# Performance work log

Measured on AMD Instinct MI355X. Metric: run time of the kernel, lower is better.

Reference implementation:

```python
import jax, jax.numpy as jnp
import numpy as np

DIM = 384; HEADS = 6; POINTS = 4; LEVELS = 3; HID = 96
B = 2; D0 = 12; H0 = 12; W0 = 12
NMID = D0 * H0 * W0          # mid-level tokens
NTOK = 73 * NMID // 8        # total tokens across 3 scales


def _ln(x, w, b, eps=1e-6):
    m = x.mean(-1, keepdims=True)
    v = ((x - m) ** 2).mean(-1, keepdims=True)
    return (x - m) * jax.lax.rsqrt(v + eps) * w + b


def _make_ref(shapes):
    # matches get_reference_points: per-level normalized centers, stacked as (d, x, y)
    refs = []
    for (D_, H_, W_) in shapes:
        d = (jnp.arange(D_, dtype=jnp.float32) + 0.5) / D_
        y = (jnp.arange(H_, dtype=jnp.float32) + 0.5) / H_
        x = (jnp.arange(W_, dtype=jnp.float32) + 0.5) / W_
        dd, yy, xx = jnp.meshgrid(d, y, x, indexing='ij')
        refs.append(jnp.stack([dd.ravel(), xx.ravel(), yy.ravel()], -1))
    return jnp.concatenate(refs, 0)[None, :, None, :]  # [1, N, 1, 3]


def _sample_level(v, D_, H_, W_, loc):
    # v: [B,S,h,hd]; loc: [B,Nq,h,P,3] normalized (d,x,y); trilinear, zero padding,
    # align_corners=False semantics (pixel = norm*size - 0.5)
    Bq, Nq, h, P, _ = loc.shape
    hd = v.shape[-1]
    pd = loc[..., 0] * D_ - 0.5
    px = loc[..., 1] * W_ - 0.5
    py = loc[..., 2] * H_ - 0.5
    d0 = jnp.floor(pd); x0 = jnp.floor(px); y0 = jnp.floor(py)
    fd = pd - d0; fx = px - x0; fy = py - y0
    d0 = d0.astype(jnp.int32); x0 = x0.astype(jnp.int32); y0 = y0.astype(jnp.int32)
    acc = jnp.zeros((Bq, Nq, h, P, hd), v.dtype)
    for dd in (0, 1):  # fixed 8-corner loop
        for dy in (0, 1):
            for dx in (0, 1):
                di = d0 + dd; yi = y0 + dy; xi = x0 + dx
                wgt = (fd if dd else 1.0 - fd) * (fy if dy else 1.0 - fy) * (fx if dx else 1.0 - fx)
                valid = ((di >= 0) & (di < D_) & (yi >= 0) & (yi < H_) & (xi >= 0) & (xi < W_)).astype(v.dtype)
                idx = (jnp.clip(di, 0, D_ - 1) * H_ + jnp.clip(yi, 0, H_ - 1)) * W_ + jnp.clip(xi, 0, W_ - 1)
                idx_t = idx.transpose(0, 1, 3, 2).reshape(Bq, Nq * P, h)
                g = jnp.take_along_axis(v, idx_t[..., None], axis=1)  # [B,Nq*P,h,hd]
                g = g.reshape(Bq, Nq, P, h, hd).transpose(0, 1, 3, 2, 4)
                acc = acc + (wgt * valid)[..., None] * g
    return acc  # [B,Nq,h,P,hd]


def _msdeform(q, ref, feat, shapes, off_w, off_b, aw_w, aw_b, val_w, val_b, out_w, out_b):
    Bq, Nq, C = q.shape
    hd = C // HEADS
    value = (feat @ val_w + val_b).reshape(Bq, -1, HEADS, hd)
    off = (q @ off_w + off_b).reshape(Bq, Nq, HEADS, LEVELS, POINTS, 3)
    aw = jax.nn.softmax((q @ aw_w + aw_b).reshape(Bq, Nq, HEADS, LEVELS * POINTS), -1)
    aw = aw.reshape(Bq, Nq, HEADS, LEVELS, POINTS)
    # offset normalizer in (d, x, y) order -> (D, W, H)
    norm = jnp.array([[D_, W_, H_] for (D_, H_, W_) in shapes], dtype=q.dtype)
    loc = ref[:, :, None, :, None, :] + off / norm[None, None, None, :, None, :]
    out = jnp.zeros((Bq, Nq, HEADS, hd), q.dtype)
    start = 0
    for l, (D_, H_, W_) in enumerate(shapes):
        S = D_ * H_ * W_
        sampled = _sample_level(value[:, start:start + S], D_, H_, W_, loc[:, :, :, l])
        out = out + jnp.einsum('bqhp,bqhpd->bqhd', aw[:, :, :, l], sampled)
        start += S
    return out.reshape(Bq, Nq, C) @ out_w + out_b


def _dwconv_seg(x, Dv, Hv, Wv, w, b):
    Bq, S, C = x.shape
    xv = x.reshape(Bq, Dv, Hv, Wv, C)
    y = jax.lax.conv_general_dilated(xv, w, (1, 1, 1), 'SAME',
                                     dimension_numbers=('NDHWC', 'DHWIO', 'NDHWC'),
                                     feature_group_count=C) + b
    return y.reshape(Bq, S, C)


def _conv_ffn(x, D, H, W, fc1_w, fc1_b, dw_w, dw_b, fc2_w, fc2_b):
    x = x @ fc1_w + fc1_b
    n = x.shape[1] // 73
    x1 = _dwconv_seg(x[:, :64 * n], 2 * D, 2 * H, 2 * W, dw_w, dw_b)
    x2 = _dwconv_seg(x[:, 64 * n:72 * n], D, H, W, dw_w, dw_b)
    x3 = _dwconv_seg(x[:, 72 * n:], D // 2, H // 2, W // 2, dw_w, dw_b)
    x = jax.nn.gelu(jnp.concatenate([x1, x2, x3], 1), approximate=False)
    return x @ fc2_w + fc2_b


def _forward(query, feat, D, H, W,
             qnorm_w, qnorm_b, fnorm_w, fnorm_b, ext_qnorm_w, ext_qnorm_b,
             ext_fnorm_w, ext_fnorm_b, ffn_norm_w, ffn_norm_b,
             off_w, off_b, aw_w, aw_b, val_w, val_b, out_w, out_b,
             fc1_w, fc1_b, dw_w, dw_b, fc2_w, fc2_b):
    n_mid = D * H * W
    n_high = 8 * n_mid
    x2 = query[:, n_high:n_high + n_mid] + feat
    q = jnp.concatenate([query[:, :n_high], x2, query[:, n_high + n_mid:]], 1)
    shapes = [(2 * D, 2 * H, 2 * W), (D, H, W), (D // 2, H // 2, W // 2)]
    ref = _make_ref(shapes)
    qn = _ln(q, qnorm_w, qnorm_b)      # CTI_toC.query_norm
    fn = _ln(q, fnorm_w, fnorm_b)      # CTI_toC.feat_norm
    aq = _ln(qn, ext_qnorm_w, ext_qnorm_b)  # MultiscaleExtractor.query_norm
    af = _ln(fn, ext_fnorm_w, ext_fnorm_b)  # MultiscaleExtractor.feat_norm
    out = qn + _msdeform(aq, ref, af, shapes, off_w, off_b, aw_w, aw_b, val_w, val_b, out_w, out_b)
    out = out + _conv_ffn(_ln(out, ffn_norm_w, ffn_norm_b), D, H, W,
                          fc1_w, fc1_b, dw_w, dw_b, fc2_w, fc2_b)
    return out


def setup_inputs() -> dict:
    key = jax.random.key(0)
    ks = jax.random.split(key, 16)
    w = lambda k, *s: jax.random.normal(k, s, jnp.float32) * 0.02
    NO = HEADS * LEVELS * POINTS * 3
    NA = HEADS * LEVELS * POINTS
    return {
        'query': jax.random.normal(ks[0], (B, NTOK, DIM), jnp.float32),
        'reference_points': jax.random.uniform(ks[1], (1, NTOK, 1, 3), dtype=jnp.float32),
        'feat': jax.random.normal(ks[2], (B, NMID, DIM), jnp.float32),
        'spatial_shapes': jnp.array([[2 * D0, 2 * H0, 2 * W0], [D0, H0, W0], [D0 // 2, H0 // 2, W0 // 2]], jnp.int32),
        'level_start_index': jnp.array([0, 8 * NMID, 9 * NMID], jnp.int32),
        'D': D0, 'H': H0, 'W': W0,
        'qnorm_w': jnp.ones(DIM), 'qnorm_b': jnp.zeros(DIM),
        'fnorm_w': jnp.ones(DIM), 'fnorm_b': jnp.zeros(DIM),
        'ext_qnorm_w': jnp.ones(DIM), 'ext_qnorm_b': jnp.zeros(DIM),
        'ext_fnorm_w': jnp.ones(DIM), 'ext_fnorm_b': jnp.zeros(DIM),
        'ffn_norm_w': jnp.ones(DIM), 'ffn_norm_b': jnp.zeros(DIM),
        'off_w': w(ks[3], DIM, NO), 'off_b': jnp.zeros(NO),
        'aw_w': w(ks[4], DIM, NA), 'aw_b': jnp.zeros(NA),
        'val_w': w(ks[5], DIM, DIM), 'val_b': jnp.zeros(DIM),
        'out_w': w(ks[6], DIM, DIM), 'out_b': jnp.zeros(DIM),
        'fc1_w': w(ks[7], DIM, HID), 'fc1_b': jnp.zeros(HID),
        'dw_w': w(ks[8], 3, 3, 3, 1, HID), 'dw_b': jnp.zeros(HID),
        'fc2_w': w(ks[9], HID, DIM), 'fc2_b': jnp.zeros(DIM),
    }


def reference(query, reference_points, feat, spatial_shapes, level_start_index, D, H, W,
              qnorm_w, qnorm_b, fnorm_w, fnorm_b, ext_qnorm_w, ext_qnorm_b,
              ext_fnorm_w, ext_fnorm_b, ffn_norm_w, ffn_norm_b,
              off_w, off_b, aw_w, aw_b, val_w, val_b, out_w, out_b,
              fc1_w, fc1_b, dw_w, dw_b, fc2_w, fc2_b):
    # reference_points / spatial_shapes / level_start_index are required by the torch
    # signature but unused: CTI_toC recomputes deform inputs internally.
    return _forward(query, feat, D, H, W,
                    qnorm_w, qnorm_b, fnorm_w, fnorm_b, ext_qnorm_w, ext_qnorm_b,
                    ext_fnorm_w, ext_fnorm_b, ffn_norm_w, ffn_norm_b,
                    off_w, off_b, aw_w, aw_b, val_w, val_b, out_w, out_b,
                    fc1_w, fc1_b, dw_w, dw_b, fc2_w, fc2_b)
```

## Files before the change

### kernel.cpp

```cpp
#include <hip/hip_runtime.h>
#include <hip/hip_fp16.h>
#include <cstdint>
#include <cstddef>

#define DIM    384
#define HEADS  6
#define HD     64
#define NTOK   15768
#define NMID   1728
#define BATCH  2
#define ROWS   (BATCH*NTOK)
#define MPAD   31616
#define L1START 13824
#define L2START 15552
#define HID    96
#define VROWS  (ROWS + 8)
#define VSLAB  ((size_t)VROWS * 64)

typedef __attribute__((ext_vector_type(8))) short short8;
typedef __attribute__((ext_vector_type(4))) float floatx4;

__device__ __forceinline__ unsigned short f2bf(float x){
  unsigned u = __float_as_uint(x);
  unsigned r = (u + 0x7FFFu + ((u >> 16) & 1u)) >> 16;
  return (unsigned short)r;
}

__device__ __forceinline__ float wave_sum(float v){
  #pragma unroll
  for (int o = 32; o; o >>= 1) v += __shfl_xor(v, o, 64);
  return v;
}

__device__ __forceinline__ void ln384(const float* x, float* y,
                                      const float* __restrict__ w,
                                      const float* __restrict__ b, int lane){
  float s = 0.f;
  #pragma unroll
  for (int j = 0; j < 6; j++) s += x[j];
  s = wave_sum(s);
  float m = s * (1.f/384.f);
  float v = 0.f;
  #pragma unroll
  for (int j = 0; j < 6; j++){ float d = x[j] - m; v += d*d; }
  v = wave_sum(v) * (1.f/384.f);
  float rs = rsqrtf(v + 1e-6f);
  #pragma unroll
  for (int j = 0; j < 6; j++){
    int c = j*64 + lane;
    y[j] = (x[j] - m) * rs * w[c] + b[c];
  }
}

__global__ void k_ln_front(const float* __restrict__ query, const float* __restrict__ feat,
                           const float* __restrict__ qw,  const float* __restrict__ qb,
                           const float* __restrict__ fw,  const float* __restrict__ fb,
                           const float* __restrict__ eqw, const float* __restrict__ eqb,
                           const float* __restrict__ efw, const float* __restrict__ efb,
                           float* __restrict__ qn, unsigned short* __restrict__ aq,
                           unsigned short* __restrict__ af){
  int wid = blockIdx.x * (blockDim.x >> 6) + (threadIdx.x >> 6);
  if (wid >= ROWS) return;
  int lane = threadIdx.x & 63;
  int b = wid / NTOK, t = wid - b*NTOK;
  const float* qp = query + (size_t)wid * DIM;
  float x[6];
  #pragma unroll
  for (int j = 0; j < 6; j++) x[j] = qp[j*64 + lane];
  if (t >= L1START && t < L2START){
    const float* fp = feat + ((size_t)b*NMID + (t - L1START)) * DIM;
    #pragma unroll
    for (int j = 0; j < 6; j++) x[j] += fp[j*64 + lane];
  }
  float y[6], z[6];
  ln384(x, y, qw, qb, lane);
  {
    float* o = qn + (size_t)wid * DIM;
    #pragma unroll
    for (int j = 0; j < 6; j++) o[j*64 + lane] = y[j];
  }
  ln384(y, z, eqw, eqb, lane);
  {
    unsigned short* o = aq + (size_t)wid * DIM;
    #pragma unroll
    for (int j = 0; j < 6; j++) o[j*64 + lane] = f2bf(z[j]);
  }
  ln384(x, y, fw, fb, lane);
  ln384(y, z, efw, efb, lane);
  {
    unsigned short* o = af + (size_t)wid * DIM;
    #pragma unroll
    for (int j = 0; j < 6; j++) o[j*64 + lane] = f2bf(z[j]);
  }
}

__global__ void k_ln(const float* __restrict__ in, const float* __restrict__ w,
                     const float* __restrict__ b, unsigned short* __restrict__ out){
  int wid = blockIdx.x * (blockDim.x >> 6) + (threadIdx.x >> 6);
  if (wid >= ROWS) return;
  int lane = threadIdx.x & 63;
  float x[6], y[6];
  const float* p = in + (size_t)wid * DIM;
  #pragma unroll
  for (int j = 0; j < 6; j++) x[j] = p[j*64 + lane];
  ln384(x, y, w, b, lane);
  unsigned short* o = out + (size_t)wid * DIM;
  #pragma unroll
  for (int j = 0; j < 6; j++) o[j*64 + lane] = f2bf(y[j]);
}

__global__ void k_cvt_all(const float* __restrict__ val_w, const float* __restrict__ off_w,
                          const float* __restrict__ aw_w,  const float* __restrict__ out_w,
                          const float* __restrict__ fc1_w, const float* __restrict__ fc2_w,
                          const float* __restrict__ off_b, const float* __restrict__ aw_b,
                          unsigned short* __restrict__ wt_val, unsigned short* __restrict__ wt_offaw,
                          unsigned short* __restrict__ wt_out, unsigned short* __restrict__ wt_fc1,
                          unsigned short* __restrict__ wt_fc2, float* __restrict__ offaw_b){
  int id = blockIdx.x * blockDim.x + threadIdx.x;
  if (id < 147456){
    int n = id / 384, k = id - n*384;
    wt_val[id] = f2bf(val_w[(size_t)k*384 + n]);
  } else if (id < 294912){
    int i = id - 147456;
    int n = i / 384, k = i - n*384;
    float v = 0.f;
    if (n < 216) v = off_w[(size_t)k*216 + n];
    else if (n >= 256 && n < 328) v = aw_w[(size_t)k*72 + (n-256)];
    wt_offaw[i] = f2bf(v);
  } else if (id < 442368){
    int i = id - 294912;
    int n = i / 384, k = i - n*384;
    wt_out[i] = f2bf(out_w[(size_t)k*384 + n]);
  } else if (id < 491520){
    int i = id - 442368;
    int n = i / 384, k = i - n*384;
    wt_fc1[i] = f2bf((n < 96) ? fc1_w[(size_t)k*96 + n] : 0.f);
  } else if (id < 528384){
    int i = id - 491520;
    int n = i / 96, k = i - n*96;
    wt_fc2[i] = f2bf(fc2_w[(size_t)k*384 + n]);
  } else if (id < 528768){
    int n = id - 528384;
    float v = 0.f;
    if (n < 216) v = off_b[n];
    else if (n >= 256 && n < 328) v = aw_b[n-256];
    offaw_b[n] = v;
  }
}

template<int OUTMODE>
__global__ __launch_bounds__(256) void k_gemm(
    const unsigned short* __restrict__ A,
    const unsigned short* __restrict__ Wt,
    const float* __restrict__ bias,
    const float* __restrict__ R,
    void* __restrict__ Cv,
    int M, int N, int K){
  __shared__ __align__(16) unsigned short As[128*32];
  __shared__ __align__(16) unsigned short Bs[128*32];
  int tid = threadIdx.x;
  int w = tid >> 6, lane = tid & 63;
  int m0 = blockIdx.y * 128, n0 = blockIdx.x * 128;
  int m_off = (w & 1) * 64, n_off = (w >> 1) * 64;

  floatx4 acc[4][4] = {};

  int sr = lane >> 2;
  int sc = (lane & 3) * 8;
  int lrow = lane & 15;
  int kq = (lane >> 4) * 8;

  for (int k0 = 0; k0 < K; k0 += 32){
    #pragma unroll
    for (int s = 0; s < 2; s++){
      int c = w * 2 + s;
      const unsigned short* ga = A  + (size_t)(m0 + c*16 + sr) * K + k0 + sc;
      __builtin_amdgcn_global_load_lds(
          (const __attribute__((address_space(1))) void*)ga,
          (__attribute__((address_space(3))) void*)(As + c*512), 16, 0, 0);
      const unsigned short* gb = Wt + (size_t)(n0 + c*16 + sr) * K + k0 + sc;
      __builtin_amdgcn_global_load_lds(
          (const __attribute__((address_space(1))) void*)gb,
          (__attribute__((address_space(3))) void*)(Bs + c*512), 16, 0, 0);
    }
    __syncthreads();
    short8 afr[4], bfr[4];
    #pragma unroll
    for (int i = 0; i < 4; i++)
      afr[i] = *(const short8*)(As + (m_off + i*16 + lrow)*32 + kq);
    #pragma unroll
    for (int j = 0; j < 4; j++)
      bfr[j] = *(const short8*)(Bs + (n_off + j*16 + lrow)*32 + kq);
    #pragma unroll
    for (int i = 0; i < 4; i++)
      #pragma unroll
      for (int j = 0; j < 4; j++)
        acc[i][j] = __builtin_amdgcn_mfma_f32_16x16x32_bf16(afr[i], bfr[j], acc[i][j], 0, 0, 0);
    __syncthreads();
  }

  int cn = n0 + n_off + lrow;
  int rbase = m0 + m_off + (lane >> 4) * 4;
  #pragma unroll
  for (int j = 0; j < 4; j++){
    int n = cn + j*16;
    if (n >= N) continue;
    float bj = bias[n];
    #pragma unroll
    for (int i = 0; i < 4; i++){
      int mb = rbase + i*16;
      #pragma unroll
      for (int r = 0; r < 4; r++){
        int m = mb + r;
        if (m < M){
          float v = acc[i][j][r] + bj;
          if (R) v += R[(size_t)m * N + n];
          if (OUTMODE == 0)      ((float*)Cv)[(size_t)m * N + n] = v;
          else if (OUTMODE == 1) ((unsigned short*)Cv)[(size_t)m * N + n] = f2bf(v);
          else {
            ((__half*)Cv)[(size_t)(n >> 6) * VSLAB + (size_t)m * 64 + (n & 63)] =
                __float2half_rn(v);
          }
        }
      }
    }
  }
}

__global__ __launch_bounds__(384) void k_msdeform(const __half* __restrict__ vt,
                                                  const float* __restrict__ offaw,
                                                  unsigned short* __restrict__ msout){
  int bx = blockIdx.x;
  int r = (bx & 7) * (ROWS/8) + (bx >> 3);
  int head = threadIdx.x >> 6;
  int lane = threadIdx.x & 63;
  int b = (r >= NTOK) ? 1 : 0;
  int t = r - b * NTOK;

  float refd, refy, refx;
  if (t < L1START){
    int i = t;
    int dd = i / 576; int rem = i - dd*576; int yy = rem / 24; int xx = rem - yy*24;
    refd = (dd + 0.5f) * (1.f/24.f); refy = (yy + 0.5f) * (1.f/24.f); refx = (xx + 0.5f) * (1.f/24.f);
  } else if (t < L2START){
    int i = t - L1START;
    int dd = i / 144; int rem = i - dd*144; int yy = rem / 12; int xx = rem - yy*12;
    refd = (dd + 0.5f) * (1.f/12.f); refy = (yy + 0.5f) * (1.f/12.f); refx = (xx + 0.5f) * (1.f/12.f);
  } else {
    int i = t - L2START;
    int dd = i / 36; int rem = i - dd*36; int yy = rem / 6; int xx = rem - yy*6;
    refd = (dd + 0.5f) * (1.f/6.f); refy = (yy + 0.5f) * (1.f/6.f); refx = (xx + 0.5f) * (1.f/6.f);
  }

  float logit = (lane < 12) ? offaw[(size_t)r * 384 + 256 + head * 12 + lane] : -1e30f;
  float mx = logit;
  mx = fmaxf(mx, __shfl_xor(mx, 1));
  mx = fmaxf(mx, __shfl_xor(mx, 2));
  mx = fmaxf(mx, __shfl_xor(mx, 4));
  mx = fmaxf(mx, __shfl_xor(mx, 8));
  float e = (lane < 12) ? __expf(logit - mx) : 0.f;
  float s = e;
  s += __shfl_xor(s, 1);
  s += __shfl_xor(s, 2);
  s += __shfl_xor(s, 4);
  s += __shfl_xor(s, 8);
  float aww = e / s;
  float awwj = __shfl(aww, lane >> 2, 64);

  int rowk = 0, wgtk = 0;
  if (lane < 48){
    int j = lane >> 2, p = lane & 3;
    int l = j >> 2;
    int Dl  = (l == 0) ? 24 : ((l == 1) ? 12 : 6);
    int lst = (l == 0) ? 0  : ((l == 1) ? L1START : L2START);
    const float* op = offaw + (size_t)r * 384 + head * 36 + j * 3;
    float od = op[0], ox = op[1], oy = op[2];
    float fDl = (float)Dl;
    float pd = refd * fDl + od - 0.5f;
    float px = refx * fDl + ox - 0.5f;
    float py = refy * fDl + oy - 0.5f;
    float fld = floorf(pd), flx = floorf(px), fly = floorf(py);
    float fd = pd - fld, fx = px - flx, fy = py - fly;
    int d0 = (int)fld, x0 = (int)flx, y0 = (int)fly;
    int cz = p >> 1, cy = p & 1;
    int di = d0 + cz, yi = y0 + cy;
    bool vzy = (di >= 0) & (di < Dl) & (yi >= 0) & (yi < Dl);
    float wz = cz ? fd : 1.f - fd;
    float wy = cy ? fy : 1.f - fy;
    float wp = vzy ? (wz * awwj) * wy : 0.f;
    int rs = min(max(x0, 0), Dl - 1);
    float wlo_x = (rs == x0) ? (1.f - fx) : ((rs == x0 + 1) ? fx : 0.f);
    float whi_x = ((rs == x0) && (x0 + 1 < Dl)) ? fx : 0.f;
    int dc = min(max(di, 0), Dl - 1);
    int yc = min(max(yi, 0), Dl - 1);
    rowk = (b * NTOK + lst) + (dc * Dl + yc) * Dl + rs;
    __half2 wh = __floats2half2_rn(wp * wlo_x, wp * whi_x);
    wgtk = *(int*)&wh;
  }

  int grp = lane >> 4;
  unsigned selperm = (lane & 8) ? 0x03020302u : 0x01000100u;
  int rowv[12]; unsigned wsel[12];
  #pragma unroll
  for (int j = 0; j < 12; j++){
    rowv[j] = __shfl(rowk, j*4 + grp, 64);
    unsigned wj = (unsigned)__shfl(wgtk, j*4 + grp, 64);
    wsel[j] = __builtin_amdgcn_perm(wj, wj, selperm);
  }

  int head_u = __builtin_amdgcn_readfirstlane(head);
  const char* vbase = (const char*)(vt + (size_t)head_u * VSLAB);
  unsigned laneoff = (unsigned)(lane & 15) << 4;

  __half2 hz; *(int*)&hz = 0;
  __half2 a0 = hz, a1 = hz, a2 = hz, a3 = hz;
  #pragma unroll
  for (int j = 0; j < 12; j++){
    unsigned off = ((unsigned)rowv[j] << 7) + laneoff;
    uint4 v = *(const uint4*)(vbase + off);
    __half2 wh = *(__half2*)&wsel[j];
    a0 = __hfma2(wh, *(__half2*)&v.x, a0);
    a1 = __hfma2(wh, *(__half2*)&v.y, a1);
    a2 = __hfma2(wh, *(__half2*)&v.z, a2);
    a3 = __hfma2(wh, *(__half2*)&v.w, a3);
  }

  int i0 = *(int*)&a0, i1 = *(int*)&a1, i2 = *(int*)&a2, i3 = *(int*)&a3;
  int p0 = __shfl_xor(i0, 8, 64); int p1 = __shfl_xor(i1, 8, 64);
  int p2 = __shfl_xor(i2, 8, 64); int p3 = __shfl_xor(i3, 8, 64);
  a0 = __hadd2(a0, *(__half2*)&p0);
  a1 = __hadd2(a1, *(__half2*)&p1);
  a2 = __hadd2(a2, *(__half2*)&p2);
  a3 = __hadd2(a3, *(__half2*)&p3);
  float2 f0 = __half22float2(a0), f1 = __half22float2(a1);
  float2 f2 = __half22float2(a2), f3 = __half22float2(a3);
  float sv[8] = {f0.x, f0.y, f1.x, f1.y, f2.x, f2.y, f3.x, f3.y};
  #pragma unroll
  for (int k = 0; k < 8; k++){
    sv[k] += __shfl_xor(sv[k], 16, 64);
    sv[k] += __shfl_xor(sv[k], 32, 64);
  }

  if (lane < 8){
    uint4 pk;
    pk.x = ((unsigned)f2bf(sv[1]) << 16) | (unsigned)f2bf(sv[0]);
    pk.y = ((unsigned)f2bf(sv[3]) << 16) | (unsigned)f2bf(sv[2]);
    pk.z = ((unsigned)f2bf(sv[5]) << 16) | (unsigned)f2bf(sv[4]);
    pk.w = ((unsigned)f2bf(sv[7]) << 16) | (unsigned)f2bf(sv[6]);
    *(uint4*)(msout + (size_t)r * DIM + head * 64 + lane * 8) = pk;
  }
}

__global__ void k_dwconv_gelu(const float* __restrict__ h, const float* __restrict__ dww,
                              const float* __restrict__ dwb, unsigned short* __restrict__ h2){
  int gid = blockIdx.x * blockDim.x + threadIdx.x;
  if (gid >= ROWS * 24) return;
  int c4 = gid % 24;
  int r = gid / 24;
  int c = c4 * 4;
  int b = (r >= NTOK) ? 1 : 0;
  int t = r - b * NTOK;
  int base, DL, i;
  if (t < L1START){ base = 0; DL = 24; i = t; }
  else if (t < L2START){ base = L1START; DL = 12; i = t - L1START; }
  else { base = L2START; DL = 6; i = t - L2START; }
  int dd, yy, xx;
  if (DL == 24){ dd = i / 576; int rem = i - dd*576; yy = rem / 24; xx = rem - yy*24; }
  else if (DL == 12){ dd = i / 144; int rem = i - dd*144; yy = rem / 12; xx = rem - yy*12; }
  else { dd = i / 36; int rem = i - dd*36; yy = rem / 6; xx = rem - yy*6; }
  float4 acc = {0.f, 0.f, 0.f, 0.f};
  #pragma unroll
  for (int kz = 0; kz < 3; kz++){
    int nd = dd + kz - 1; if (nd < 0 || nd >= DL) continue;
    #pragma unroll
    for (int ky = 0; ky < 3; ky++){
      int ny = yy + ky - 1; if (ny < 0 || ny >= DL) continue;
      #pragma unroll
      for (int kx = 0; kx < 3; kx++){
        int nx = xx + kx - 1; if (nx < 0 || nx >= DL) continue;
        int nt = base + (nd * DL + ny) * DL + nx;
        float4 hv = *(const float4*)(h + ((size_t)(b*NTOK + nt)) * HID + c);
        float4 wv = *(const float4*)(dww + (size_t)((kz*3 + ky)*3 + kx) * HID + c);
        acc.x += hv.x * wv.x; acc.y += hv.y * wv.y;
        acc.z += hv.z * wv.z; acc.w += hv.w * wv.w;
      }
    }
  }
  float4 bv = *(const float4*)(dwb + c);
  acc.x += bv.x; acc.y += bv.y; acc.z += bv.z; acc.w += bv.w;
  const float k = 0.70710678118654752440f;
  float g0 = 0.5f * acc.x * (1.f + erff(acc.x * k));
  float g1 = 0.5f * acc.y * (1.f + erff(acc.y * k));
  float g2 = 0.5f * acc.z * (1.f + erff(acc.z * k));
  float g3 = 0.5f * acc.w * (1.f + erff(acc.w * k));
  uint2 pk;
  pk.x = ((unsigned)f2bf(g1) << 16) | (unsigned)f2bf(g0);
  pk.y = ((unsigned)f2bf(g3) << 16) | (unsigned)f2bf(g2);
  *(uint2*)(h2 + (size_t)r * HID + c) = pk;
}

extern "C" void kernel_launch(void* const* d_in, const int* in_sizes, int n_in,
                              void* d_out, int out_size, void* d_ws, size_t ws_size,
                              hipStream_t stream){
  const float* query = (const float*)d_in[0];
  const float* feat  = (const float*)d_in[2];
  const float* qnw = (const float*)d_in[8],  *qnb = (const float*)d_in[9];
  const float* fnw = (const float*)d_in[10], *fnb = (const float*)d_in[11];
  const float* eqw = (const float*)d_in[12], *eqb = (const float*)d_in[13];
  const float* efw = (const float*)d_in[14], *efb = (const float*)d_in[15];
  const float* ffw = (const float*)d_in[16], *ffb = (const float*)d_in[17];
  const float* off_w = (const float*)d_in[18], *off_b = (const float*)d_in[19];
  const float* aw_w  = (const float*)d_in[20], *aw_b  = (const float*)d_in[21];
  const float* val_w = (const float*)d_in[22], *val_b = (const float*)d_in[23];
  const float* out_w = (const float*)d_in[24], *out_b = (const float*)d_in[25];
  const float* fc1_w = (const float*)d_in[26], *fc1_b = (const float*)d_in[27];
  const float* dw_w  = (const float*)d_in[28], *dw_b  = (const float*)d_in[29];
  const float* fc2_w = (const float*)d_in[30], *fc2_b = (const float*)d_in[31];
  float* out = (float*)d_out;

  char* p = (char*)d_ws;
  float* qn             = (float*)p;          p += (size_t)ROWS*384*4;
  unsigned short* aq    = (unsigned short*)p; p += (size_t)MPAD*384*2;
  unsigned short* af    = (unsigned short*)p; p += (size_t)MPAD*384*2;
  __half* value_t       = (__half*)p;         p += (size_t)HEADS*VSLAB*2;
  float* offaw          = (float*)p;          p += (size_t)ROWS*384*4;
  unsigned short* wt_val   = (unsigned short*)p; p += (size_t)384*384*2;
  unsigned short* wt_offaw = (unsigned short*)p; p += (size_t)384*384*2;
  unsigned short* wt_out   = (unsigned short*)p; p += (size_t)384*384*2;
  unsigned short* wt_fc1   = (unsigned short*)p; p += (size_t)128*384*2;
  unsigned short* wt_fc2   = (unsigned short*)p; p += (size_t)384*96*2;
  float* offaw_b           = (float*)p;          p += (size_t)384*4;
  unsigned short* t_buf  = aq;
  unsigned short* msout  = af;
  float* y1              = offaw;
  float* h_buf           = (float*)value_t;
  unsigned short* h2_buf = (unsigned short*)qn;

  k_cvt_all<<<(528768 + 255)/256, 256, 0, stream>>>(val_w, off_w, aw_w, out_w, fc1_w, fc2_w,
                                                    off_b, aw_b,
                                                    wt_val, wt_offaw, wt_out, wt_fc1, wt_fc2,
                                                    offaw_b);

  int lnBlocks = ROWS / 4;
  k_ln_front<<<lnBlocks, 256, 0, stream>>>(query, feat, qnw, qnb, fnw, fnb,
                                           eqw, eqb, efw, efb, qn, aq, af);

  dim3 gN384(3, MPAD/128), gN128(1, MPAD/128);

  k_gemm<2><<<gN384, 256, 0, stream>>>(af, wt_val, val_b, nullptr, value_t, ROWS, 384, 384);
  k_gemm<0><<<gN384, 256, 0, stream>>>(aq, wt_offaw, offaw_b, nullptr, offaw, ROWS, 384, 384);
  k_msdeform<<<ROWS, 384, 0, stream>>>(value_t, offaw, msout);
  k_gemm<0><<<gN384, 256, 0, stream>>>(msout, wt_out, out_b, qn, y1, ROWS, 384, 384);
  k_ln<<<lnBlocks, 256, 0, stream>>>(y1, ffw, ffb, t_buf);
  k_gemm<0><<<gN128, 256, 0, stream>>>(t_buf, wt_fc1, fc1_b, nullptr, h_buf, ROWS, 96, 384);
  k_dwconv_gelu<<<(ROWS * 24 + 255)/256, 256, 0, stream>>>(h_buf, dw_w, dw_b, h2_buf);
  k_gemm<0><<<gN384, 256, 0, stream>>>(h2_buf, wt_fc2, fc2_b, y1, out, ROWS, 384, 96);
}
```

Measured before the change: 511.5 us.

## Restructure deformable sampling to one wave per head-row with swizzle-broadcast gathers

The deformable attention kernel changes from one 384-thread block per row to 64-thread blocks indexed by (head, row). Each lane now computes one sample point and corner, so the per-lane softmax shuffle goes away. Row indices and weights are broadcast with ds_swizzle, and all 12 gathers are issued up front before the FMAs. Packed bf16 conversion uses the v_cvt_pk_bf16_f32 instruction. The weight-convert kernel now zero-fills the value padding rows. The row interleaving used for locality is dropped, and the grid gets many more small blocks.

```diff
diff --git a/kernel.cpp b/kernel.cpp
--- a/kernel.cpp
+++ b/kernel.cpp
@@ -26,6 +26,12 @@
   return (unsigned short)r;
 }
 
+__device__ __forceinline__ unsigned cvt_pk_bf16(float lo, float hi){
+  unsigned r;
+  asm("v_cvt_pk_bf16_f32 %0, %1, %2" : "=v"(r) : "v"(lo), "v"(hi));
+  return r;
+}
+
 __device__ __forceinline__ float wave_sum(float v){
   #pragma unroll
   for (int o = 32; o; o >>= 1) v += __shfl_xor(v, o, 64);
@@ -115,7 +121,8 @@
                           const float* __restrict__ off_b, const float* __restrict__ aw_b,
                           unsigned short* __restrict__ wt_val, unsigned short* __restrict__ wt_offaw,
                           unsigned short* __restrict__ wt_out, unsigned short* __restrict__ wt_fc1,
-                          unsigned short* __restrict__ wt_fc2, float* __restrict__ offaw_b){
+                          unsigned short* __restrict__ wt_fc2, float* __restrict__ offaw_b,
+                          unsigned short* __restrict__ vt_pad){
   int id = blockIdx.x * blockDim.x + threadIdx.x;
   if (id < 147456){
     int n = id / 384, k = id - n*384;
@@ -145,6 +152,10 @@
     if (n < 216) v = off_b[n];
     else if (n >= 256 && n < 328) v = aw_b[n-256];
     offaw_b[n] = v;
+  } else if (id < 531840){
+    int i = id - 528768;
+    int hh = i >> 9, rem = i & 511;
+    vt_pad[(size_t)hh * VSLAB + (size_t)ROWS * 64 + rem] = 0;
   }
 }
 
@@ -227,12 +238,11 @@
   }
 }
 
-__global__ __launch_bounds__(384) void k_msdeform(const __half* __restrict__ vt,
-                                                  const float* __restrict__ offaw,
-                                                  unsigned short* __restrict__ msout){
-  int bx = blockIdx.x;
-  int r = (bx & 7) * (ROWS/8) + (bx >> 3);
-  int head = threadIdx.x >> 6;
+__global__ __launch_bounds__(64, 4) void k_msdeform(const __half* __restrict__ vt,
+                                                    const float* __restrict__ offaw,
+                                                    unsigned short* __restrict__ msout){
+  int head = blockIdx.x;
+  int r    = blockIdx.y;
   int lane = threadIdx.x & 63;
   int b = (r >= NTOK) ? 1 : 0;
   int t = r - b * NTOK;
@@ -252,24 +262,26 @@
     refd = (dd + 0.5f) * (1.f/6.f); refy = (yy + 0.5f) * (1.f/6.f); refx = (xx + 0.5f) * (1.f/6.f);
   }
 
-  float logit = (lane < 12) ? offaw[(size_t)r * 384 + 256 + head * 12 + lane] : -1e30f;
+  int s   = lane & 15;
+  int grp = lane >> 4;
+
+  float logit = (s < 12) ? offaw[(size_t)r * 384 + 256 + head * 12 + s] : -1e30f;
   float mx = logit;
-  mx = fmaxf(mx, __shfl_xor(mx, 1));
-  mx = fmaxf(mx, __shfl_xor(mx, 2));
-  mx = fmaxf(mx, __shfl_xor(mx, 4));
-  mx = fmaxf(mx, __shfl_xor(mx, 8));
-  float e = (lane < 12) ? __expf(logit - mx) : 0.f;
-  float s = e;
-  s += __shfl_xor(s, 1);
-  s += __shfl_xor(s, 2);
-  s += __shfl_xor(s, 4);
-  s += __shfl_xor(s, 8);
-  float aww = e / s;
-  float awwj = __shfl(aww, lane >> 2, 64);
+  mx = fmaxf(mx, __shfl_xor(mx, 1, 64));
+  mx = fmaxf(mx, __shfl_xor(mx, 2, 64));
+  mx = fmaxf(mx, __shfl_xor(mx, 4, 64));
+  mx = fmaxf(mx, __shfl_xor(mx, 8, 64));
+  float e = (s < 12) ? __expf(logit - mx) : 0.f;
+  float sum = e;
+  sum += __shfl_xor(sum, 1, 64);
+  sum += __shfl_xor(sum, 2, 64);
+  sum += __shfl_xor(sum, 4, 64);
+  sum += __shfl_xor(sum, 8, 64);
+  float aww = e / sum;
 
   int rowk = 0, wgtk = 0;
-  if (lane < 48){
-    int j = lane >> 2, p = lane & 3;
+  if (s < 12){
+    int j = s;
     int l = j >> 2;
     int Dl  = (l == 0) ? 24 : ((l == 1) ? 12 : 6);
     int lst = (l == 0) ? 0  : ((l == 1) ? L1START : L2START);
@@ -282,12 +294,12 @@
     float fld = floorf(pd), flx = floorf(px), fly = floorf(py);
     float fd = pd - fld, fx = px - flx, fy = py - fly;
     int d0 = (int)fld, x0 = (int)flx, y0 = (int)fly;
-    int cz = p >> 1, cy = p & 1;
+    int cz = grp >> 1, cy = grp & 1;
     int di = d0 + cz, yi = y0 + cy;
     bool vzy = (di >= 0) & (di < Dl) & (yi >= 0) & (yi < Dl);
     float wz = cz ? fd : 1.f - fd;
     float wy = cy ? fy : 1.f - fy;
-    float wp = vzy ? (wz * awwj) * wy : 0.f;
+    float wp = vzy ? (wz * aww) * wy : 0.f;
     int rs = min(max(x0, 0), Dl - 1);
     float wlo_x = (rs == x0) ? (1.f - fx) : ((rs == x0 + 1) ? fx : 0.f);
     float whi_x = ((rs == x0) && (x0 + 1 < Dl)) ? fx : 0.f;
@@ -298,27 +310,30 @@
     wgtk = *(int*)&wh;
   }
 
-  int grp = lane >> 4;
+  const char* vbase = (const char*)(vt + (size_t)head * VSLAB);
+  unsigned laneoff = (unsigned)(lane & 15) << 4;
   unsigned selperm = (lane & 8) ? 0x03020302u : 0x01000100u;
-  int rowv[12]; unsigned wsel[12];
-  #pragma unroll
-  for (int j = 0; j < 12; j++){
-    rowv[j] = __shfl(rowk, j*4 + grp, 64);
-    unsigned wj = (unsigned)__shfl(wgtk, j*4 + grp, 64);
-    wsel[j] = __builtin_amdgcn_perm(wj, wj, selperm);
-  }
-
-  int head_u = __builtin_amdgcn_readfirstlane(head);
-  const char* vbase = (const char*)(vt + (size_t)head_u * VSLAB);
-  unsigned laneoff = (unsigned)(lane & 15) << 4;
+
+  uint4 vd[12]; unsigned wv[12];
+  #define MS_LOAD(J) { int rw_ = __builtin_amdgcn_ds_swizzle(rowk, ((J) << 5) | 16); \
+    vd[J] = *(const uint4*)(vbase + ((((unsigned)rw_) << 7) + laneoff)); }
+  MS_LOAD(0)  MS_LOAD(1)  MS_LOAD(2)  MS_LOAD(3)
+  MS_LOAD(4)  MS_LOAD(5)  MS_LOAD(6)  MS_LOAD(7)
+  MS_LOAD(8)  MS_LOAD(9)  MS_LOAD(10) MS_LOAD(11)
+  #undef MS_LOAD
+  #define MS_W(J) { unsigned wj_ = (unsigned)__builtin_amdgcn_ds_swizzle(wgtk, ((J) << 5) | 16); \
+    wv[J] = __builtin_amdgcn_perm(wj_, wj_, selperm); }
+  MS_W(0)  MS_W(1)  MS_W(2)  MS_W(3)
+  MS_W(4)  MS_W(5)  MS_W(6)  MS_W(7)
+  MS_W(8)  MS_W(9)  MS_W(10) MS_W(11)
+  #undef MS_W
 
   __half2 hz; *(int*)&hz = 0;
   __half2 a0 = hz, a1 = hz, a2 = hz, a3 = hz;
   #pragma unroll
   for (int j = 0; j < 12; j++){
-    unsigned off = ((unsigned)rowv[j] << 7) + laneoff;
-    uint4 v = *(const uint4*)(vbase + off);
-    __half2 wh = *(__half2*)&wsel[j];
+    __half2 wh = *(__half2*)&wv[j];
+    uint4 v = vd[j];
     a0 = __hfma2(wh, *(__half2*)&v.x, a0);
     a1 = __hfma2(wh, *(__half2*)&v.y, a1);
     a2 = __hfma2(wh, *(__half2*)&v.z, a2);
@@ -343,10 +358,10 @@
 
   if (lane < 8){
     uint4 pk;
-    pk.x = ((unsigned)f2bf(sv[1]) << 16) | (unsigned)f2bf(sv[0]);
-    pk.y = ((unsigned)f2bf(sv[3]) << 16) | (unsigned)f2bf(sv[2]);
-    pk.z = ((unsigned)f2bf(sv[5]) << 16) | (unsigned)f2bf(sv[4]);
-    pk.w = ((unsigned)f2bf(sv[7]) << 16) | (unsigned)f2bf(sv[6]);
+    pk.x = cvt_pk_bf16(sv[0], sv[1]);
+    pk.y = cvt_pk_bf16(sv[2], sv[3]);
+    pk.z = cvt_pk_bf16(sv[4], sv[5]);
+    pk.w = cvt_pk_bf16(sv[6], sv[7]);
     *(uint4*)(msout + (size_t)r * DIM + head * 64 + lane * 8) = pk;
   }
 }
@@ -436,10 +451,10 @@
   float* h_buf           = (float*)value_t;
   unsigned short* h2_buf = (unsigned short*)qn;
 
-  k_cvt_all<<<(528768 + 255)/256, 256, 0, stream>>>(val_w, off_w, aw_w, out_w, fc1_w, fc2_w,
+  k_cvt_all<<<(531840 + 255)/256, 256, 0, stream>>>(val_w, off_w, aw_w, out_w, fc1_w, fc2_w,
                                                     off_b, aw_b,
                                                     wt_val, wt_offaw, wt_out, wt_fc1, wt_fc2,
-                                                    offaw_b);
+                                                    offaw_b, (unsigned short*)value_t);
 
   int lnBlocks = ROWS / 4;
   k_ln_front<<<lnBlocks, 256, 0, stream>>>(query, feat, qnw, qnb, fnw, fnb,
@@ -449,7 +464,7 @@
 
   k_gemm<2><<<gN384, 256, 0, stream>>>(af, wt_val, val_b, nullptr, value_t, ROWS, 384, 384);
   k_gemm<0><<<gN384, 256, 0, stream>>>(aq, wt_offaw, offaw_b, nullptr, offaw, ROWS, 384, 384);
-  k_msdeform<<<ROWS, 384, 0, stream>>>(value_t, offaw, msout);
+  k_msdeform<<<dim3(HEADS, ROWS), 64, 0, stream>>>(value_t, offaw, msout);
   k_gemm<0><<<gN384, 256, 0, stream>>>(msout, wt_out, out_b, qn, y1, ROWS, 384, 384);
   k_ln<<<lnBlocks, 256, 0, stream>>>(y1, ffw, ffb, t_buf);
   k_gemm<0><<<gN128, 256, 0, stream>>>(t_buf, wt_fc1, fc1_b, nullptr, h_buf, ROWS, 96, 384);
```

New measurement: 488.0 us. -4.6%, faster.
